# Kernel optimization log

Measured on AMD Instinct MI355X. Metric: run time of the kernel, lower is better.

## Reference

```python
import jax, jax.numpy as jnp
import numpy as np

# FP4 lookup table (E2M1-style values) exactly as in FP4Codec.FP4_TABLE
FP4_TABLE = jnp.array([0.0, 0.5, 1.0, 1.5, 2.0, 3.0, 4.0, 6.0,
                       0.0, -0.5, -1.0, -1.5, -2.0, -3.0, -4.0, -6.0],
                      dtype=jnp.float32)

M, K, N = 128, 4096, 16384


def setup_inputs() -> dict:
    key = jax.random.key(0)
    k1, k2, k3, k4 = jax.random.split(key, 4)
    x = jax.random.normal(k1, (M, K), dtype=jnp.float32)
    # packed bytes: each int holds two 4-bit FP4 indices (hi<<4 | lo)
    weight_fp4 = jax.random.randint(k2, (N, K // 2), 0, 256, dtype=jnp.int32)
    # positive per-output-channel scale (encode guarantees >= 1e-8)
    weight_scale = jax.random.uniform(k3, (N,), dtype=jnp.float32,
                                      minval=1e-3, maxval=2e-2)
    bias = jax.random.normal(k4, (N,), dtype=jnp.float32) * 0.02
    return {"x": x, "weight_fp4": weight_fp4,
            "weight_scale": weight_scale, "bias": bias}


def _dequantize(weight_fp4, weight_scale):
    p = weight_fp4.astype(jnp.uint8)
    hi = (p >> 4) & 0xF
    lo = p & 0xF
    # interleave [hi, lo] along last dim -> [N, K] indices
    idx = jnp.stack([hi, lo], axis=-1).reshape(p.shape[0], -1)
    return FP4_TABLE[idx] * weight_scale[:, None]  # [N, K] fp32


def reference(x, weight_fp4, weight_scale, bias):
    w = _dequantize(weight_fp4, weight_scale)          # [N, K]
    y = jnp.einsum('mk,nk->mn', x, w) + bias            # [M, N]
    return jax.nn.gelu(y, approximate=False)            # exact GELU like F.gelu
```

## Files before the change

### kernel.cpp

```cpp
#include <hip/hip_runtime.h>
#include <stdint.h>


#define M_DIM 128
#define K_DIM 4096
#define N_DIM 16384
#define BN    64
#define BK    64
#define NK    (K_DIM/BK)
#define NT    512
#define NBLK  (N_DIM/BN)

#define A_BYTES 16384
#define B_BYTES 8192
#define NBUF    4
#define AOFF(b) ((b)*A_BYTES)
#define BOFF(b) (NBUF*A_BYTES + (b)*B_BYTES)
#define LDS_SZ  (NBUF*(A_BYTES+B_BYTES))

typedef __attribute__((ext_vector_type(8))) __bf16 bf16x8;
typedef __attribute__((ext_vector_type(4))) float  f32x4;
typedef unsigned short ushort_t;

__device__ __forceinline__ unsigned f2b_bits(float f) {
  unsigned u = __builtin_bit_cast(unsigned, f);
  u += 0x7FFFu + ((u >> 16) & 1u);
  return u >> 16;
}

__global__ void convert_x_kernel(const float* __restrict__ x,
                                 ushort_t* __restrict__ xb) {
  int i = (blockIdx.x * blockDim.x + threadIdx.x) * 4;
  float4 v = *(const float4*)(x + i);
  ushort4 p;
  p.x = (ushort_t)f2b_bits(v.x);
  p.y = (ushort_t)f2b_bits(v.y);
  p.z = (ushort_t)f2b_bits(v.z);
  p.w = (ushort_t)f2b_bits(v.w);
  *(ushort4*)(xb + i) = p;
}

__device__ __forceinline__ void gl16(const void* g, void* l) {
  __builtin_amdgcn_global_load_lds(
      (const __attribute__((address_space(1))) void*)g,
      (__attribute__((address_space(3))) void*)l, 16, 0, 0);
}

__device__ __forceinline__ bf16x8 decode8(uint4 p) {
  unsigned u01 = __builtin_amdgcn_perm(p.y, p.x, 0x04000400u);
  unsigned u23 = __builtin_amdgcn_perm(p.w, p.z, 0x04000400u);
  unsigned q   = __builtin_amdgcn_perm(u23, u01, 0x05040100u);
  unsigned e  = (q >> 4) & 0x0F0F0F0Fu;
  unsigned o  = q & 0x0F0F0F0Fu;
  unsigned em = e & 0x07070707u, om = o & 0x07070707u;
  unsigned elo = __builtin_amdgcn_perm(0xC0804000u, 0xC0800000u, em);
  unsigned ehi = __builtin_amdgcn_perm(0x40404040u, 0x3F3F3F00u, em);
  unsigned olo = __builtin_amdgcn_perm(0xC0804000u, 0xC0800000u, om);
  unsigned ohi = __builtin_amdgcn_perm(0x40404040u, 0x3F3F3F00u, om);
  ehi |= (e & 0x08080808u) << 4;
  ohi |= (o & 0x08080808u) << 4;
  unsigned t0 = __builtin_amdgcn_perm(ehi, elo, 0x05010400u);
  unsigned t1 = __builtin_amdgcn_perm(ohi, olo, 0x05010400u);
  unsigned t2 = __builtin_amdgcn_perm(ehi, elo, 0x07030602u);
  unsigned t3 = __builtin_amdgcn_perm(ohi, olo, 0x07030602u);
  uint4 r;
  r.x = __builtin_amdgcn_perm(t1, t0, 0x05040100u);
  r.y = __builtin_amdgcn_perm(t1, t0, 0x07060302u);
  r.z = __builtin_amdgcn_perm(t3, t2, 0x05040100u);
  r.w = __builtin_amdgcn_perm(t3, t2, 0x07060302u);
  return __builtin_bit_cast(bf16x8, r);
}

#define MFMA16(a_, b_, c_) __builtin_amdgcn_mfma_f32_16x16x32_bf16(a_, b_, c_, 0, 0, 0)

template<bool USE_XB>
__global__ __launch_bounds__(NT) void fp4gemm_kernel(
    const void* __restrict__ xsrc,
    const int*  __restrict__ wq,
    const float* __restrict__ scale,
    const float* __restrict__ bias,
    float* __restrict__ out) {
  __shared__ __align__(16) uint8_t lds[LDS_SZ];

  const int t   = threadIdx.x;
  const int w   = t >> 6;
  const int l   = t & 63;
  const int l16 = l & 15;
  const int lq  = l >> 4;
  const int mq  = w >> 1;
  const int nh  = w & 1;

  const int bid = blockIdx.x;
  const int n0  = ((bid & 7) * (NBLK / 8) + (bid >> 3)) * BN;

  const int srow = t >> 3;
  const int scol = (t & 7) * 16;
  const int sswz = (srow & 7) << 4;
  const int scbs = scol ^ sswz;
  const int bwr  = srow * 128 + (scol ^ sswz);

  const uint8_t* xb  = (const uint8_t*)xsrc;
  const uint8_t* wqb = (const uint8_t*)wq;

  uint4 rs0, rs1, rs2, rs3;

#define ISSUE_A(k_, b_) do { \
  gl16(xb + (size_t)(srow) * 8192 + (size_t)(k_) * 128 + scbs, \
       lds + AOFF(b_) + w * 1024); \
  gl16(xb + (size_t)(64 + srow) * 8192 + (size_t)(k_) * 128 + scbs, \
       lds + AOFF(b_) + 8192 + w * 1024); \
} while (0)

#define ISSUE_B(k_, s_) do { \
  rs##s_ = *(const uint4*)(wqb + (size_t)(n0 + srow) * 8192 + (size_t)(k_) * 128 + scol); \
} while (0)

#define DECODE_B(s_, b_) do { \
  *(bf16x8*)(lds + BOFF(b_) + bwr) = decode8(rs##s_); \
} while (0)

#define WAITV(N_) asm volatile("s_waitcnt vmcnt(" #N_ ")" ::: "memory")
#define BARRIER() do { \
  asm volatile("s_waitcnt lgkmcnt(0)" ::: "memory"); \
  __builtin_amdgcn_s_barrier(); \
  __builtin_amdgcn_sched_barrier(0); \
} while (0)

  f32x4 acc00 = {0,0,0,0}, acc01 = {0,0,0,0};
  f32x4 acc10 = {0,0,0,0}, acc11 = {0,0,0,0};

  const int cBase = (lq << 4) ^ ((l16 & 7) << 4);
  const int aR0 = (mq * 32 + l16) * 128;
  const int bR0 = (nh * 32 + l16) * 128;

#define COMPUTE(b_) do { \
  const uint8_t* Ab_ = lds + AOFF(b_); \
  const uint8_t* Bb_ = lds + BOFF(b_); \
  _Pragma("unroll") \
  for (int ks_ = 0; ks_ < 2; ++ks_) { \
    const int cS_ = (ks_ << 6) ^ cBase; \
    bf16x8 a0_ = *(const bf16x8*)(Ab_ + aR0 + cS_); \
    bf16x8 a1_ = *(const bf16x8*)(Ab_ + aR0 + 2048 + cS_); \
    bf16x8 b0_ = *(const bf16x8*)(Bb_ + bR0 + cS_); \
    bf16x8 b1_ = *(const bf16x8*)(Bb_ + bR0 + 2048 + cS_); \
    acc00 = MFMA16(a0_, b0_, acc00); \
    acc01 = MFMA16(a0_, b1_, acc01); \
    acc10 = MFMA16(a1_, b0_, acc10); \
    acc11 = MFMA16(a1_, b1_, acc11); \
  } \
} while (0)

#define BODY(k_, u_, cb_) do { \
  ISSUE_A((k_) + 2, u_); \
  WAITV(6); \
  BARRIER(); \
  DECODE_B(u_, u_); \
  ISSUE_B((k_) + 6, u_); \
  COMPUTE(cb_); \
} while (0)

  if constexpr (USE_XB) {
    ISSUE_B(0, 0); ISSUE_B(1, 1); ISSUE_B(2, 2); ISSUE_B(3, 3);
    ISSUE_A(0, 0); ISSUE_A(1, 1);
    WAITV(4);
    DECODE_B(0, 0); DECODE_B(1, 1);
    ISSUE_B(4, 0); ISSUE_B(5, 1);
    ISSUE_A(2, 2); WAITV(6); BARRIER();
    DECODE_B(2, 2); ISSUE_B(6, 2); COMPUTE(0);
    ISSUE_A(3, 3); WAITV(7); BARRIER();
    DECODE_B(3, 3); ISSUE_B(7, 3); COMPUTE(1);
    for (int j = 0; j < 14; ++j) {
      const int kt = 2 + 4 * j;
      BODY(kt + 0, 0, 2);
      BODY(kt + 1, 1, 3);
      BODY(kt + 2, 2, 0);
      BODY(kt + 3, 3, 1);
    }
    ISSUE_A(60, 0); WAITV(6); BARRIER(); DECODE_B(0, 0); COMPUTE(2);
    ISSUE_A(61, 1); WAITV(5); BARRIER(); DECODE_B(1, 1); COMPUTE(3);
    ISSUE_A(62, 2); WAITV(4); BARRIER(); DECODE_B(2, 2); COMPUTE(0);
    ISSUE_A(63, 3); WAITV(4); BARRIER(); DECODE_B(3, 3); COMPUTE(1);
    WAITV(2); BARRIER(); COMPUTE(2);
    WAITV(0); BARRIER(); COMPUTE(3);
  } else {
    for (int kt = 0; kt < NK; ++kt) {
      __syncthreads();
#pragma unroll
      for (int i = 0; i < 2; ++i) {
        const float* xf = (const float*)xsrc +
            (size_t)(i * 64 + srow) * K_DIM + (size_t)kt * BK + (scol >> 1);
        float4 v0 = *(const float4*)(xf);
        float4 v1 = *(const float4*)(xf + 4);
        uint4 pk = make_uint4(f2b_bits(v0.x) | (f2b_bits(v0.y) << 16),
                              f2b_bits(v0.z) | (f2b_bits(v0.w) << 16),
                              f2b_bits(v1.x) | (f2b_bits(v1.y) << 16),
                              f2b_bits(v1.z) | (f2b_bits(v1.w) << 16));
        *(uint4*)(lds + AOFF(kt & 1) + (size_t)(i * 64 + srow) * 128 +
                  (scol ^ sswz)) = pk;
      }
      {
        uint4 pv = *(const uint4*)(wqb + (size_t)(n0 + srow) * 8192 +
                                   (size_t)kt * 128 + scol);
        *(bf16x8*)(lds + BOFF(kt & 1) + bwr) = decode8(pv);
      }
      __syncthreads();
      COMPUTE(kt & 1);
    }
  }

  const int ng = n0 + nh * 32 + l16;
#pragma unroll
  for (int ni = 0; ni < 2; ++ni) {
    const int ngc = ng + ni * 16;
    const float s  = scale[ngc];
    const float bb = bias[ngc];
    f32x4 v0 = ni ? acc01 : acc00;
    f32x4 v1 = ni ? acc11 : acc10;
#pragma unroll
    for (int mi = 0; mi < 2; ++mi) {
      f32x4 vv = mi ? v1 : v0;
#pragma unroll
      for (int j = 0; j < 4; ++j) {
        int m = mq * 32 + mi * 16 + lq * 4 + j;
        float y = vv[j] * s + bb;
        float g = 0.5f * y * (1.0f + erff(y * 0.70710678118654752f));
        out[(size_t)m * N_DIM + ngc] = g;
      }
    }
  }
#undef ISSUE_A
#undef ISSUE_B
#undef DECODE_B
#undef WAITV
#undef BARRIER
#undef COMPUTE
#undef BODY
}

extern "C" void kernel_launch(void* const* d_in, const int* in_sizes, int n_in,
                              void* d_out, int out_size, void* d_ws, size_t ws_size,
                              hipStream_t stream) {
  const float* x     = (const float*)d_in[0];
  const int*   wq    = (const int*)d_in[1];
  const float* scale = (const float*)d_in[2];
  const float* bias  = (const float*)d_in[3];
  float* out = (float*)d_out;

  const size_t xb_bytes = (size_t)M_DIM * K_DIM * sizeof(ushort_t);
  if (ws_size >= xb_bytes) {
    ushort_t* xb = (ushort_t*)d_ws;
    convert_x_kernel<<<(M_DIM * K_DIM) / (256 * 4), 256, 0, stream>>>(x, xb);
    fp4gemm_kernel<true><<<NBLK, NT, 0, stream>>>(xb, wq, scale, bias, out);
  } else {
    fp4gemm_kernel<false><<<NBLK, NT, 0, stream>>>(x, wq, scale, bias, out);
  }
}
```

Before: 42.14 us.

## Pre-compact int32 FP4 weights into byte-packed workspace before GEMM

Adds a pre-pass kernel that packs the int32-per-byte weight array into a dense byte array in workspace. The GEMM then loads 4 bytes per thread instead of 16 and decodes directly, cutting weight bytes read inside the GEMM. The cost is an extra kernel that reads the full int32 weights and writes the packed copy on every call, raising total memory traffic.

```diff
diff --git a/kernel.cpp b/kernel.cpp
--- a/kernel.cpp
+++ b/kernel.cpp
@@ -5,6 +5,7 @@
 #define M_DIM 128
 #define K_DIM 4096
 #define N_DIM 16384
+#define KP    (K_DIM/2)
 #define BN    64
 #define BK    64
 #define NK    (K_DIM/BK)
@@ -18,6 +19,9 @@
 #define BOFF(b) (NBUF*A_BYTES + (b)*B_BYTES)
 #define LDS_SZ  (NBUF*(A_BYTES+B_BYTES))
 
+#define XB_BYTES  ((size_t)M_DIM * K_DIM * 2)
+#define WPK_BYTES ((size_t)N_DIM * KP)
+
 typedef __attribute__((ext_vector_type(8))) __bf16 bf16x8;
 typedef __attribute__((ext_vector_type(4))) float  f32x4;
 typedef unsigned short ushort_t;
@@ -28,8 +32,8 @@
   return u >> 16;
 }
 
-__global__ void convert_x_kernel(const float* __restrict__ x,
-                                 ushort_t* __restrict__ xb) {
+__global__ __launch_bounds__(256) void convert_x_kernel(
+    const float* __restrict__ x, ushort_t* __restrict__ xb) {
   int i = (blockIdx.x * blockDim.x + threadIdx.x) * 4;
   float4 v = *(const float4*)(x + i);
   ushort4 p;
@@ -40,16 +44,29 @@
   *(ushort4*)(xb + i) = p;
 }
 
+__device__ __forceinline__ unsigned pack4(uint4 p) {
+  unsigned u01 = __builtin_amdgcn_perm(p.y, p.x, 0x04000400u);
+  unsigned u23 = __builtin_amdgcn_perm(p.w, p.z, 0x04000400u);
+  return __builtin_amdgcn_perm(u23, u01, 0x05040100u);
+}
+
+__global__ __launch_bounds__(256) void compact_w_kernel(
+    const int* __restrict__ wq, uint8_t* __restrict__ wpk) {
+  size_t idx = (size_t)blockIdx.x * 256 + threadIdx.x;
+  const uint4* s = (const uint4*)wq + idx * 4;
+  uint4 a = s[0], b = s[1], c = s[2], d = s[3];
+  uint4 o;
+  o.x = pack4(a); o.y = pack4(b); o.z = pack4(c); o.w = pack4(d);
+  ((uint4*)wpk)[idx] = o;
+}
+
 __device__ __forceinline__ void gl16(const void* g, void* l) {
   __builtin_amdgcn_global_load_lds(
       (const __attribute__((address_space(1))) void*)g,
       (__attribute__((address_space(3))) void*)l, 16, 0, 0);
 }
 
-__device__ __forceinline__ bf16x8 decode8(uint4 p) {
-  unsigned u01 = __builtin_amdgcn_perm(p.y, p.x, 0x04000400u);
-  unsigned u23 = __builtin_amdgcn_perm(p.w, p.z, 0x04000400u);
-  unsigned q   = __builtin_amdgcn_perm(u23, u01, 0x05040100u);
+__device__ __forceinline__ bf16x8 decode4(unsigned q) {
   unsigned e  = (q >> 4) & 0x0F0F0F0Fu;
   unsigned o  = q & 0x0F0F0F0Fu;
   unsigned em = e & 0x07070707u, om = o & 0x07070707u;
@@ -71,12 +88,14 @@
   return __builtin_bit_cast(bf16x8, r);
 }
 
+__device__ __forceinline__ bf16x8 decode8(uint4 p) { return decode4(pack4(p)); }
+
 #define MFMA16(a_, b_, c_) __builtin_amdgcn_mfma_f32_16x16x32_bf16(a_, b_, c_, 0, 0, 0)
 
-template<bool USE_XB>
+template<int MODE>
 __global__ __launch_bounds__(NT) void fp4gemm_kernel(
     const void* __restrict__ xsrc,
-    const int*  __restrict__ wq,
+    const void* __restrict__ wsrc,
     const float* __restrict__ scale,
     const float* __restrict__ bias,
     float* __restrict__ out) {
@@ -100,9 +119,11 @@
   const int bwr  = srow * 128 + (scol ^ sswz);
 
   const uint8_t* xb  = (const uint8_t*)xsrc;
-  const uint8_t* wqb = (const uint8_t*)wq;
-
-  uint4 rs0, rs1, rs2, rs3;
+  const uint8_t* wqb = (const uint8_t*)wsrc;
+  const uint8_t* wpk = (const uint8_t*)wsrc;
+
+  unsigned rs0, rs1, rs2, rs3;
+  uint4    rq0, rq1, rq2, rq3;
 
 #define ISSUE_A(k_, b_) do { \
   gl16(xb + (size_t)(srow) * 8192 + (size_t)(k_) * 128 + scbs, \
@@ -112,11 +133,20 @@
 } while (0)
 
 #define ISSUE_B(k_, s_) do { \
-  rs##s_ = *(const uint4*)(wqb + (size_t)(n0 + srow) * 8192 + (size_t)(k_) * 128 + scol); \
+  if constexpr (MODE == 2) { \
+    rs##s_ = *(const unsigned*)(wpk + (size_t)(n0 + srow) * KP + \
+                                (size_t)(k_) * 32 + (t & 7) * 4); \
+  } else { \
+    rq##s_ = *(const uint4*)(wqb + (size_t)(n0 + srow) * 8192 + \
+                             (size_t)(k_) * 128 + scol); \
+  } \
 } while (0)
 
 #define DECODE_B(s_, b_) do { \
-  *(bf16x8*)(lds + BOFF(b_) + bwr) = decode8(rs##s_); \
+  bf16x8 dv_; \
+  if constexpr (MODE == 2) dv_ = decode4(rs##s_); \
+  else                     dv_ = decode8(rq##s_); \
+  *(bf16x8*)(lds + BOFF(b_) + bwr) = dv_; \
 } while (0)
 
 #define WAITV(N_) asm volatile("s_waitcnt vmcnt(" #N_ ")" ::: "memory")
@@ -159,7 +189,7 @@
   COMPUTE(cb_); \
 } while (0)
 
-  if constexpr (USE_XB) {
+  if constexpr (MODE >= 1) {
     ISSUE_B(0, 0); ISSUE_B(1, 1); ISSUE_B(2, 2); ISSUE_B(3, 3);
     ISSUE_A(0, 0); ISSUE_A(1, 1);
     WAITV(4);
@@ -246,12 +276,17 @@
   const float* bias  = (const float*)d_in[3];
   float* out = (float*)d_out;
 
-  const size_t xb_bytes = (size_t)M_DIM * K_DIM * sizeof(ushort_t);
-  if (ws_size >= xb_bytes) {
+  if (ws_size >= XB_BYTES + WPK_BYTES) {
+    ushort_t* xb  = (ushort_t*)d_ws;
+    uint8_t*  wpk = (uint8_t*)d_ws + XB_BYTES;
+    convert_x_kernel<<<(M_DIM * K_DIM) / (256 * 4), 256, 0, stream>>>(x, xb);
+    compact_w_kernel<<<(int)(WPK_BYTES / (256 * 16)), 256, 0, stream>>>(wq, wpk);
+    fp4gemm_kernel<2><<<NBLK, NT, 0, stream>>>(xb, wpk, scale, bias, out);
+  } else if (ws_size >= XB_BYTES) {
     ushort_t* xb = (ushort_t*)d_ws;
     convert_x_kernel<<<(M_DIM * K_DIM) / (256 * 4), 256, 0, stream>>>(x, xb);
-    fp4gemm_kernel<true><<<NBLK, NT, 0, stream>>>(xb, wq, scale, bias, out);
+    fp4gemm_kernel<1><<<NBLK, NT, 0, stream>>>(xb, wq, scale, bias, out);
   } else {
-    fp4gemm_kernel<false><<<NBLK, NT, 0, stream>>>(x, wq, scale, bias, out);
+    fp4gemm_kernel<0><<<NBLK, NT, 0, stream>>>(x, wq, scale, bias, out);
   }
 }
```

Result: slower. 61.83 us (+46.7%).

## Split K across wave halves with LDS reduction and retime A prefetch

Applied to the files above, without the earlier changes.

Changes the wave-to-tile mapping: each wave now covers a 64x32 output sub-tile over half of each BK slice (split-K across two wave groups). Partial sums are reduced through LDS before the GELU epilogue. This reduces redundant LDS fragment loads per MFMA, since B fragments are reused across four A rows. The A global-to-LDS prefetch is also issued after the barrier and one stage further ahead. The cost is an extra LDS reduction, more accumulator registers, and only half the waves running the epilogue.

```diff
diff --git a/kernel.cpp b/kernel.cpp
--- a/kernel.cpp
+++ b/kernel.cpp
@@ -28,8 +28,8 @@
   return u >> 16;
 }
 
-__global__ void convert_x_kernel(const float* __restrict__ x,
-                                 ushort_t* __restrict__ xb) {
+__global__ __launch_bounds__(256) void convert_x_kernel(
+    const float* __restrict__ x, ushort_t* __restrict__ xb) {
   int i = (blockIdx.x * blockDim.x + threadIdx.x) * 4;
   float4 v = *(const float4*)(x + i);
   ushort4 p;
@@ -87,7 +87,8 @@
   const int l   = t & 63;
   const int l16 = l & 15;
   const int lq  = l >> 4;
-  const int mq  = w >> 1;
+  const int kh  = w >> 2;
+  const int mh  = (w >> 1) & 1;
   const int nh  = w & 1;
 
   const int bid = blockIdx.x;
@@ -102,7 +103,7 @@
   const uint8_t* xb  = (const uint8_t*)xsrc;
   const uint8_t* wqb = (const uint8_t*)wq;
 
-  uint4 rs0, rs1, rs2, rs3;
+  uint4 rq0, rq1, rq2, rq3;
 
 #define ISSUE_A(k_, b_) do { \
   gl16(xb + (size_t)(srow) * 8192 + (size_t)(k_) * 128 + scbs, \
@@ -112,11 +113,12 @@
 } while (0)
 
 #define ISSUE_B(k_, s_) do { \
-  rs##s_ = *(const uint4*)(wqb + (size_t)(n0 + srow) * 8192 + (size_t)(k_) * 128 + scol); \
+  rq##s_ = *(const uint4*)(wqb + (size_t)(n0 + srow) * 8192 + \
+                           (size_t)(k_) * 128 + scol); \
 } while (0)
 
 #define DECODE_B(s_, b_) do { \
-  *(bf16x8*)(lds + BOFF(b_) + bwr) = decode8(rs##s_); \
+  *(bf16x8*)(lds + BOFF(b_) + bwr) = decode8(rq##s_); \
 } while (0)
 
 #define WAITV(N_) asm volatile("s_waitcnt vmcnt(" #N_ ")" ::: "memory")
@@ -126,60 +128,55 @@
   __builtin_amdgcn_sched_barrier(0); \
 } while (0)
 
-  f32x4 acc00 = {0,0,0,0}, acc01 = {0,0,0,0};
-  f32x4 acc10 = {0,0,0,0}, acc11 = {0,0,0,0};
-
-  const int cBase = (lq << 4) ^ ((l16 & 7) << 4);
-  const int aR0 = (mq * 32 + l16) * 128;
+  f32x4 acc[4][2] = {{{0,0,0,0},{0,0,0,0}},{{0,0,0,0},{0,0,0,0}},
+                     {{0,0,0,0},{0,0,0,0}},{{0,0,0,0},{0,0,0,0}}};
+
+  const int cS  = ((lq << 4) + (kh << 6)) ^ ((l16 & 7) << 4);
+  const int aR0 = (mh * 64 + l16) * 128;
   const int bR0 = (nh * 32 + l16) * 128;
 
 #define COMPUTE(b_) do { \
   const uint8_t* Ab_ = lds + AOFF(b_); \
   const uint8_t* Bb_ = lds + BOFF(b_); \
+  bf16x8 bf0_ = *(const bf16x8*)(Bb_ + bR0 + cS); \
+  bf16x8 bf1_ = *(const bf16x8*)(Bb_ + bR0 + 2048 + cS); \
   _Pragma("unroll") \
-  for (int ks_ = 0; ks_ < 2; ++ks_) { \
-    const int cS_ = (ks_ << 6) ^ cBase; \
-    bf16x8 a0_ = *(const bf16x8*)(Ab_ + aR0 + cS_); \
-    bf16x8 a1_ = *(const bf16x8*)(Ab_ + aR0 + 2048 + cS_); \
-    bf16x8 b0_ = *(const bf16x8*)(Bb_ + bR0 + cS_); \
-    bf16x8 b1_ = *(const bf16x8*)(Bb_ + bR0 + 2048 + cS_); \
-    acc00 = MFMA16(a0_, b0_, acc00); \
-    acc01 = MFMA16(a0_, b1_, acc01); \
-    acc10 = MFMA16(a1_, b0_, acc10); \
-    acc11 = MFMA16(a1_, b1_, acc11); \
+  for (int r_ = 0; r_ < 4; ++r_) { \
+    bf16x8 af_ = *(const bf16x8*)(Ab_ + aR0 + r_ * 2048 + cS); \
+    acc[r_][0] = MFMA16(af_, bf0_, acc[r_][0]); \
+    acc[r_][1] = MFMA16(af_, bf1_, acc[r_][1]); \
   } \
 } while (0)
 
-#define BODY(k_, u_, cb_) do { \
-  ISSUE_A((k_) + 2, u_); \
+#define BODY(k_, u_, ab_, cb_) do { \
   WAITV(6); \
   BARRIER(); \
   DECODE_B(u_, u_); \
   ISSUE_B((k_) + 6, u_); \
+  ISSUE_A((k_) + 3, ab_); \
   COMPUTE(cb_); \
 } while (0)
 
   if constexpr (USE_XB) {
     ISSUE_B(0, 0); ISSUE_B(1, 1); ISSUE_B(2, 2); ISSUE_B(3, 3);
-    ISSUE_A(0, 0); ISSUE_A(1, 1);
-    WAITV(4);
+    ISSUE_A(0, 0); ISSUE_A(1, 1); ISSUE_A(2, 2);
+    WAITV(6);
     DECODE_B(0, 0); DECODE_B(1, 1);
     ISSUE_B(4, 0); ISSUE_B(5, 1);
-    ISSUE_A(2, 2); WAITV(6); BARRIER();
-    DECODE_B(2, 2); ISSUE_B(6, 2); COMPUTE(0);
-    ISSUE_A(3, 3); WAITV(7); BARRIER();
-    DECODE_B(3, 3); ISSUE_B(7, 3); COMPUTE(1);
+    WAITV(6); BARRIER();
+    DECODE_B(2, 2); ISSUE_B(6, 2); ISSUE_A(3, 3); COMPUTE(0);
+    WAITV(6); BARRIER();
+    DECODE_B(3, 3); ISSUE_B(7, 3); ISSUE_A(4, 0); COMPUTE(1);
     for (int j = 0; j < 14; ++j) {
-      const int kt = 2 + 4 * j;
-      BODY(kt + 0, 0, 2);
-      BODY(kt + 1, 1, 3);
-      BODY(kt + 2, 2, 0);
-      BODY(kt + 3, 3, 1);
-    }
-    ISSUE_A(60, 0); WAITV(6); BARRIER(); DECODE_B(0, 0); COMPUTE(2);
-    ISSUE_A(61, 1); WAITV(5); BARRIER(); DECODE_B(1, 1); COMPUTE(3);
-    ISSUE_A(62, 2); WAITV(4); BARRIER(); DECODE_B(2, 2); COMPUTE(0);
-    ISSUE_A(63, 3); WAITV(4); BARRIER(); DECODE_B(3, 3); COMPUTE(1);
+      BODY(2 + 4 * j, 0, 1, 2);
+      BODY(3 + 4 * j, 1, 2, 3);
+      BODY(4 + 4 * j, 2, 3, 0);
+      BODY(5 + 4 * j, 3, 0, 1);
+    }
+    WAITV(6); BARRIER(); DECODE_B(0, 0); ISSUE_A(61, 1); COMPUTE(2);
+    WAITV(5); BARRIER(); DECODE_B(1, 1); ISSUE_A(62, 2); COMPUTE(3);
+    WAITV(4); BARRIER(); DECODE_B(2, 2); ISSUE_A(63, 3); COMPUTE(0);
+    WAITV(4); BARRIER(); DECODE_B(3, 3); COMPUTE(1);
     WAITV(2); BARRIER(); COMPUTE(2);
     WAITV(0); BARRIER(); COMPUTE(3);
   } else {
@@ -208,23 +205,40 @@
     }
   }
 
-  const int ng = n0 + nh * 32 + l16;
-#pragma unroll
-  for (int ni = 0; ni < 2; ++ni) {
-    const int ngc = ng + ni * 16;
-    const float s  = scale[ngc];
-    const float bb = bias[ngc];
-    f32x4 v0 = ni ? acc01 : acc00;
-    f32x4 v1 = ni ? acc11 : acc10;
-#pragma unroll
-    for (int mi = 0; mi < 2; ++mi) {
-      f32x4 vv = mi ? v1 : v0;
-#pragma unroll
-      for (int j = 0; j < 4; ++j) {
-        int m = mq * 32 + mi * 16 + lq * 4 + j;
-        float y = vv[j] * s + bb;
-        float g = 0.5f * y * (1.0f + erff(y * 0.70710678118654752f));
-        out[(size_t)m * N_DIM + ngc] = g;
+  __syncthreads();
+  {
+    uint8_t* red = lds;
+    const int pos = w & 3;
+    if (w >= 4) {
+#pragma unroll
+      for (int r = 0; r < 4; ++r)
+#pragma unroll
+        for (int c = 0; c < 2; ++c)
+          *(f32x4*)(red + pos * 8192 + (r * 2 + c) * 1024 + l * 16) = acc[r][c];
+    }
+    __syncthreads();
+    if (w < 4) {
+#pragma unroll
+      for (int r = 0; r < 4; ++r)
+#pragma unroll
+        for (int c = 0; c < 2; ++c)
+          acc[r][c] += *(const f32x4*)(red + pos * 8192 + (r * 2 + c) * 1024 + l * 16);
+
+#pragma unroll
+      for (int c = 0; c < 2; ++c) {
+        const int ngc = n0 + nh * 32 + c * 16 + l16;
+        const float s  = scale[ngc];
+        const float bb = bias[ngc];
+#pragma unroll
+        for (int r = 0; r < 4; ++r) {
+#pragma unroll
+          for (int j = 0; j < 4; ++j) {
+            int m = mh * 64 + r * 16 + lq * 4 + j;
+            float y = acc[r][c][j] * s + bb;
+            float g = 0.5f * y * (1.0f + erff(y * 0.70710678118654752f));
+            out[(size_t)m * N_DIM + ngc] = g;
+          }
+        }
       }
     }
   }
@@ -246,7 +260,7 @@
   const float* bias  = (const float*)d_in[3];
   float* out = (float*)d_out;
 
-  const size_t xb_bytes = (size_t)M_DIM * K_DIM * sizeof(ushort_t);
+  const size_t xb_bytes = (size_t)M_DIM * K_DIM * 2;
   if (ws_size >= xb_bytes) {
     ushort_t* xb = (ushort_t*)d_ws;
     convert_x_kernel<<<(M_DIM * K_DIM) / (256 * 4), 256, 0, stream>>>(x, xb);
```

Measured after the change: 41.78 us (median of 2 runs). About the same (-0.8%).

## Split M across two blocks with 256-thread blocks and deeper A prefetch

Applied to the files above, without the earlier changes.

Each block now covers 64 rows of M instead of 128, using 256 threads, so the grid doubles to 512 blocks. Block pairs sharing an N tile are mapped to the same XCD to encourage L2 reuse of weight reads. Each thread now loads and decodes two weight rows, and the A prefetch distance grows from 2 to 3 stages. The aim is finer scheduling and better overlap. The cost is that every FP4 weight tile is fetched and decoded twice, which adds pressure on a memory-bound weight stream.

```diff
diff --git a/kernel.cpp b/kernel.cpp
--- a/kernel.cpp
+++ b/kernel.cpp
@@ -8,10 +8,10 @@
 #define BN    64
 #define BK    64
 #define NK    (K_DIM/BK)
-#define NT    512
-#define NBLK  (N_DIM/BN)
-
-#define A_BYTES 16384
+#define NT    256
+#define NBLK  512
+
+#define A_BYTES 8192
 #define B_BYTES 8192
 #define NBUF    4
 #define AOFF(b) ((b)*A_BYTES)
@@ -28,8 +28,8 @@
   return u >> 16;
 }
 
-__global__ void convert_x_kernel(const float* __restrict__ x,
-                                 ushort_t* __restrict__ xb) {
+__global__ __launch_bounds__(256) void convert_x_kernel(
+    const float* __restrict__ x, ushort_t* __restrict__ xb) {
   int i = (blockIdx.x * blockDim.x + threadIdx.x) * 4;
   float4 v = *(const float4*)(x + i);
   ushort4 p;
@@ -87,36 +87,43 @@
   const int l   = t & 63;
   const int l16 = l & 15;
   const int lq  = l >> 4;
-  const int mq  = w >> 1;
+  const int mq2 = w >> 1;
   const int nh  = w & 1;
 
-  const int bid = blockIdx.x;
-  const int n0  = ((bid & 7) * (NBLK / 8) + (bid >> 3)) * BN;
-
-  const int srow = t >> 3;
+  const int bid  = blockIdx.x;
+  const int n0   = ((bid & 7) * 32 + (bid >> 4)) * BN;
+  const int mblk = (bid >> 3) & 1;
+
+  const int r0   = t >> 3;
   const int scol = (t & 7) * 16;
-  const int sswz = (srow & 7) << 4;
-  const int scbs = scol ^ sswz;
-  const int bwr  = srow * 128 + (scol ^ sswz);
+  const int swz0 = (r0 & 7) << 4;
+  const int scbs = scol ^ swz0;
+  const int bwr0 = r0 * 128 + (scol ^ swz0);
+  const int bwr1 = bwr0 + 32 * 128;
 
   const uint8_t* xb  = (const uint8_t*)xsrc;
   const uint8_t* wqb = (const uint8_t*)wq;
-
-  uint4 rs0, rs1, rs2, rs3;
+  const size_t aRowBase = (size_t)(mblk * 64) * 8192;
+
+  uint4 rq0a, rq0b, rq1a, rq1b, rq2a, rq2b, rq3a, rq3b;
 
 #define ISSUE_A(k_, b_) do { \
-  gl16(xb + (size_t)(srow) * 8192 + (size_t)(k_) * 128 + scbs, \
+  gl16(xb + aRowBase + (size_t)(r0) * 8192 + (size_t)(k_) * 128 + scbs, \
        lds + AOFF(b_) + w * 1024); \
-  gl16(xb + (size_t)(64 + srow) * 8192 + (size_t)(k_) * 128 + scbs, \
-       lds + AOFF(b_) + 8192 + w * 1024); \
+  gl16(xb + aRowBase + (size_t)(32 + r0) * 8192 + (size_t)(k_) * 128 + scbs, \
+       lds + AOFF(b_) + 4096 + w * 1024); \
 } while (0)
 
 #define ISSUE_B(k_, s_) do { \
-  rs##s_ = *(const uint4*)(wqb + (size_t)(n0 + srow) * 8192 + (size_t)(k_) * 128 + scol); \
-} while (0)
-
-#define DECODE_B(s_, b_) do { \
-  *(bf16x8*)(lds + BOFF(b_) + bwr) = decode8(rs##s_); \
+  rq##s_##a = *(const uint4*)(wqb + (size_t)(n0 + r0) * 8192 + \
+                              (size_t)(k_) * 128 + scol); \
+  rq##s_##b = *(const uint4*)(wqb + (size_t)(n0 + 32 + r0) * 8192 + \
+                              (size_t)(k_) * 128 + scol); \
+} while (0)
+
+#define DECODE_B(s_) do { \
+  *(bf16x8*)(lds + BOFF(s_) + bwr0) = decode8(rq##s_##a); \
+  *(bf16x8*)(lds + BOFF(s_) + bwr1) = decode8(rq##s_##b); \
 } while (0)
 
 #define WAITV(N_) asm volatile("s_waitcnt vmcnt(" #N_ ")" ::: "memory")
@@ -129,16 +136,16 @@
   f32x4 acc00 = {0,0,0,0}, acc01 = {0,0,0,0};
   f32x4 acc10 = {0,0,0,0}, acc11 = {0,0,0,0};
 
-  const int cBase = (lq << 4) ^ ((l16 & 7) << 4);
-  const int aR0 = (mq * 32 + l16) * 128;
-  const int bR0 = (nh * 32 + l16) * 128;
+  const int aR0 = (mq2 * 32 + l16) * 128;
+  const int bR0 = (nh  * 32 + l16) * 128;
+  const int cB  = (lq << 4) ^ ((l16 & 7) << 4);
 
 #define COMPUTE(b_) do { \
   const uint8_t* Ab_ = lds + AOFF(b_); \
   const uint8_t* Bb_ = lds + BOFF(b_); \
   _Pragma("unroll") \
   for (int ks_ = 0; ks_ < 2; ++ks_) { \
-    const int cS_ = (ks_ << 6) ^ cBase; \
+    const int cS_ = (ks_ << 6) ^ cB; \
     bf16x8 a0_ = *(const bf16x8*)(Ab_ + aR0 + cS_); \
     bf16x8 a1_ = *(const bf16x8*)(Ab_ + aR0 + 2048 + cS_); \
     bf16x8 b0_ = *(const bf16x8*)(Bb_ + bR0 + cS_); \
@@ -150,78 +157,83 @@
   } \
 } while (0)
 
-#define BODY(k_, u_, cb_) do { \
-  ISSUE_A((k_) + 2, u_); \
-  WAITV(6); \
+#define BODY(k_, s_, ab_, cb_) do { \
+  WAITV(8); \
   BARRIER(); \
-  DECODE_B(u_, u_); \
-  ISSUE_B((k_) + 6, u_); \
+  DECODE_B(s_); \
+  ISSUE_B((k_) + 6, s_); \
+  ISSUE_A((k_) + 3, ab_); \
   COMPUTE(cb_); \
 } while (0)
 
   if constexpr (USE_XB) {
     ISSUE_B(0, 0); ISSUE_B(1, 1); ISSUE_B(2, 2); ISSUE_B(3, 3);
-    ISSUE_A(0, 0); ISSUE_A(1, 1);
-    WAITV(4);
-    DECODE_B(0, 0); DECODE_B(1, 1);
+    ISSUE_A(0, 0); ISSUE_A(1, 1); ISSUE_A(2, 2);
+    WAITV(6);
+    DECODE_B(0); DECODE_B(1);
     ISSUE_B(4, 0); ISSUE_B(5, 1);
-    ISSUE_A(2, 2); WAITV(6); BARRIER();
-    DECODE_B(2, 2); ISSUE_B(6, 2); COMPUTE(0);
-    ISSUE_A(3, 3); WAITV(7); BARRIER();
-    DECODE_B(3, 3); ISSUE_B(7, 3); COMPUTE(1);
-    for (int j = 0; j < 14; ++j) {
-      const int kt = 2 + 4 * j;
-      BODY(kt + 0, 0, 2);
-      BODY(kt + 1, 1, 3);
-      BODY(kt + 2, 2, 0);
-      BODY(kt + 3, 3, 1);
+    WAITV(8);  BARRIER(); DECODE_B(2); ISSUE_B(6, 2); ISSUE_A(3, 3); COMPUTE(0);
+    WAITV(10); BARRIER(); DECODE_B(3); ISSUE_B(7, 3); ISSUE_A(4, 0); COMPUTE(1);
+    WAITV(10); BARRIER(); DECODE_B(0); ISSUE_B(8, 0); ISSUE_A(5, 1); COMPUTE(2);
+    BODY(3, 1, 2, 3);
+    BODY(4, 2, 3, 0);
+    BODY(5, 3, 0, 1);
+    for (int j = 0; j < 13; ++j) {
+      const int kt = 6 + 4 * j;
+      BODY(kt + 0, 0, 1, 2);
+      BODY(kt + 1, 1, 2, 3);
+      BODY(kt + 2, 2, 3, 0);
+      BODY(kt + 3, 3, 0, 1);
     }
-    ISSUE_A(60, 0); WAITV(6); BARRIER(); DECODE_B(0, 0); COMPUTE(2);
-    ISSUE_A(61, 1); WAITV(5); BARRIER(); DECODE_B(1, 1); COMPUTE(3);
-    ISSUE_A(62, 2); WAITV(4); BARRIER(); DECODE_B(2, 2); COMPUTE(0);
-    ISSUE_A(63, 3); WAITV(4); BARRIER(); DECODE_B(3, 3); COMPUTE(1);
+    WAITV(8); BARRIER(); DECODE_B(0); ISSUE_A(61, 1); COMPUTE(2);
+    WAITV(6); BARRIER(); DECODE_B(1); ISSUE_A(62, 2); COMPUTE(3);
+    WAITV(4); BARRIER(); DECODE_B(2); ISSUE_A(63, 3); COMPUTE(0);
+    WAITV(4); BARRIER(); DECODE_B(3); COMPUTE(1);
     WAITV(2); BARRIER(); COMPUTE(2);
     WAITV(0); BARRIER(); COMPUTE(3);
   } else {
     for (int kt = 0; kt < NK; ++kt) {
       __syncthreads();
-#pragma unroll
-      for (int i = 0; i < 2; ++i) {
-        const float* xf = (const float*)xsrc +
-            (size_t)(i * 64 + srow) * K_DIM + (size_t)kt * BK + (scol >> 1);
-        float4 v0 = *(const float4*)(xf);
-        float4 v1 = *(const float4*)(xf + 4);
-        uint4 pk = make_uint4(f2b_bits(v0.x) | (f2b_bits(v0.y) << 16),
-                              f2b_bits(v0.z) | (f2b_bits(v0.w) << 16),
-                              f2b_bits(v1.x) | (f2b_bits(v1.y) << 16),
-                              f2b_bits(v1.z) | (f2b_bits(v1.w) << 16));
-        *(uint4*)(lds + AOFF(kt & 1) + (size_t)(i * 64 + srow) * 128 +
-                  (scol ^ sswz)) = pk;
-      }
       {
-        uint4 pv = *(const uint4*)(wqb + (size_t)(n0 + srow) * 8192 +
+#pragma unroll
+        for (int i = 0; i < 2; ++i) {
+          const float* xf = (const float*)xsrc +
+              (size_t)(mblk * 64 + i * 32 + r0) * K_DIM + (size_t)kt * BK +
+              (scol >> 1);
+          float4 v0 = *(const float4*)(xf);
+          float4 v1 = *(const float4*)(xf + 4);
+          uint4 pk = make_uint4(f2b_bits(v0.x) | (f2b_bits(v0.y) << 16),
+                                f2b_bits(v0.z) | (f2b_bits(v0.w) << 16),
+                                f2b_bits(v1.x) | (f2b_bits(v1.y) << 16),
+                                f2b_bits(v1.z) | (f2b_bits(v1.w) << 16));
+          *(uint4*)(lds + AOFF(kt & 1) + (size_t)(i * 32 + r0) * 128 +
+                    (scol ^ swz0)) = pk;
+        }
+        uint4 pa = *(const uint4*)(wqb + (size_t)(n0 + r0) * 8192 +
                                    (size_t)kt * 128 + scol);
-        *(bf16x8*)(lds + BOFF(kt & 1) + bwr) = decode8(pv);
+        uint4 pb = *(const uint4*)(wqb + (size_t)(n0 + 32 + r0) * 8192 +
+                                   (size_t)kt * 128 + scol);
+        *(bf16x8*)(lds + BOFF(kt & 1) + bwr0) = decode8(pa);
+        *(bf16x8*)(lds + BOFF(kt & 1) + bwr1) = decode8(pb);
       }
       __syncthreads();
       COMPUTE(kt & 1);
     }
   }
 
-  const int ng = n0 + nh * 32 + l16;
-#pragma unroll
-  for (int ni = 0; ni < 2; ++ni) {
-    const int ngc = ng + ni * 16;
+#pragma unroll
+  for (int c = 0; c < 2; ++c) {
+    const int ngc = n0 + nh * 32 + c * 16 + l16;
     const float s  = scale[ngc];
     const float bb = bias[ngc];
-    f32x4 v0 = ni ? acc01 : acc00;
-    f32x4 v1 = ni ? acc11 : acc10;
-#pragma unroll
-    for (int mi = 0; mi < 2; ++mi) {
-      f32x4 vv = mi ? v1 : v0;
+    f32x4 v0 = c ? acc01 : acc00;
+    f32x4 v1 = c ? acc11 : acc10;
+#pragma unroll
+    for (int fr = 0; fr < 2; ++fr) {
+      f32x4 vv = fr ? v1 : v0;
 #pragma unroll
       for (int j = 0; j < 4; ++j) {
-        int m = mq * 32 + mi * 16 + lq * 4 + j;
+        int m = mblk * 64 + mq2 * 32 + fr * 16 + lq * 4 + j;
         float y = vv[j] * s + bb;
         float g = 0.5f * y * (1.0f + erff(y * 0.70710678118654752f));
         out[(size_t)m * N_DIM + ngc] = g;
@@ -246,7 +258,7 @@
   const float* bias  = (const float*)d_in[3];
   float* out = (float*)d_out;
 
-  const size_t xb_bytes = (size_t)M_DIM * K_DIM * sizeof(ushort_t);
+  const size_t xb_bytes = (size_t)M_DIM * K_DIM * 2;
   if (ws_size >= xb_bytes) {
     ushort_t* xb = (ushort_t*)d_ws;
     convert_x_kernel<<<(M_DIM * K_DIM) / (256 * 4), 256, 0, stream>>>(x, xb);
```

New measurement: 44.91 us. 6.6% more time.
